# Optimization experiments

Hardware: AMD Instinct MI355X
Metric: run time of the kernel (lower is better)

Reference implementation:

```python
import jax, jax.numpy as jnp
import numpy as np

N, D_IN, H, L, K, Q = 131072, 384, 256, 32, 512, 4


def _lin_init(key, fan_in, fan_out):
    s = 1.0 / np.sqrt(fan_in)
    kw, kb = jax.random.split(key)
    w = jax.random.uniform(kw, (fan_in, fan_out), minval=-s, maxval=s, dtype=jnp.float32)
    b = jax.random.uniform(kb, (fan_out,), minval=-s, maxval=s, dtype=jnp.float32)
    return w, b


def setup_inputs() -> dict:
    key = jax.random.key(0)
    ks = jax.random.split(key, 8)
    enc_w1, enc_b1 = _lin_init(ks[1], D_IN, H)
    enc_w2, enc_b2 = _lin_init(ks[2], H, H)
    enc_w3, enc_b3 = _lin_init(ks[3], H, L)
    dec_w1, dec_b1 = _lin_init(ks[4], L, H)
    dec_w2, dec_b2 = _lin_init(ks[5], H, H)
    dec_w3, dec_b3 = _lin_init(ks[6], H, D_IN)
    codebooks = jax.random.normal(ks[7], (Q, K, L), dtype=jnp.float32) * 0.02
    x = jax.random.normal(ks[0], (N, D_IN), dtype=jnp.float32)
    return dict(x=x,
                enc_w1=enc_w1, enc_b1=enc_b1, enc_w2=enc_w2, enc_b2=enc_b2,
                enc_w3=enc_w3, enc_b3=enc_b3,
                dec_w1=dec_w1, dec_b1=dec_b1, dec_w2=dec_w2, dec_b2=dec_b2,
                dec_w3=dec_w3, dec_b3=dec_b3,
                codebooks=codebooks)


def _encoder(x, w1, b1, w2, b2, w3, b3):
    h = jax.nn.relu(x @ w1 + b1)
    h = jax.nn.relu(h @ w2 + b2)
    return h @ w3 + b3


def _decoder(z, w1, b1, w2, b2, w3, b3):
    h = jax.nn.relu(z @ w1 + b1)
    h = jax.nn.relu(h @ w2 + b2)
    return h @ w3 + b3


def _residual_vq(z, codebooks):
    """Residual VQ: Q stages of nearest-codeword lookup on the running residual.
    Returns (z_quantized with straight-through, indices [N,Q], commitment loss)."""
    residual = z
    quant_sum = jnp.zeros_like(z)
    indices = []
    commit = jnp.float32(0.0)
    for q in range(codebooks.shape[0]):  # small fixed loop over quantizer stages
        cb = codebooks[q]  # [K, L]
        # squared L2 distances [N, K] via expansion (cdist + argmin)
        d = (jnp.sum(residual * residual, axis=-1, keepdims=True)
             - 2.0 * residual @ cb.T
             + jnp.sum(cb * cb, axis=-1))
        idx = jnp.argmin(d, axis=-1)          # [N]
        qv = cb[idx]                          # gather [N, L]
        commit = commit + jnp.mean((jax.lax.stop_gradient(qv) - residual) ** 2)
        quant_sum = quant_sum + qv
        residual = residual - jax.lax.stop_gradient(qv)
        indices.append(idx)
    # straight-through estimator
    z_q = z + jax.lax.stop_gradient(quant_sum - z)
    return z_q, jnp.stack(indices, axis=-1), commit


def reference(x, enc_w1, enc_b1, enc_w2, enc_b2, enc_w3, enc_b3,
              dec_w1, dec_b1, dec_w2, dec_b2, dec_w3, dec_b3, codebooks):
    z = _encoder(x, enc_w1, enc_b1, enc_w2, enc_b2, enc_w3, enc_b3)
    z_q, indices, commit = _residual_vq(z, codebooks)
    x_recon = _decoder(z_q, dec_w1, dec_b1, dec_w2, dec_b2, dec_w3, dec_b3)
    return x_recon, indices, commit
```

## Files before the change

### kernel.cpp

```cpp
#include <hip/hip_runtime.h>
#include <hip/hip_bf16.h>
#include <math.h>


#define N_ROWS 131072
#define D_IN   384
#define H_DIM  256
#define L_DIM  32
#define K_CB   512
#define Q_ST   4
#define VQ_ROWS 256
#define NPART  (N_ROWS / VQ_ROWS)

typedef __attribute__((ext_vector_type(8))) short short8v;
typedef __attribute__((ext_vector_type(4))) float f32x4;

__device__ __forceinline__ ushort f2bf(float v)
{
    __hip_bfloat16 b = __float2bfloat16(v);
    return *reinterpret_cast<ushort*>(&b);
}

__device__ __forceinline__ float np_sumsq32(const float* __restrict__ v)
{
    #pragma clang fp contract(off)
    float s0 = v[0]*v[0], s1 = v[1]*v[1], s2 = v[2]*v[2], s3 = v[3]*v[3];
    float s4 = v[4]*v[4], s5 = v[5]*v[5], s6 = v[6]*v[6], s7 = v[7]*v[7];
    s0 = s0 + v[8]*v[8];   s1 = s1 + v[9]*v[9];   s2 = s2 + v[10]*v[10]; s3 = s3 + v[11]*v[11];
    s4 = s4 + v[12]*v[12]; s5 = s5 + v[13]*v[13]; s6 = s6 + v[14]*v[14]; s7 = s7 + v[15]*v[15];
    s0 = s0 + v[16]*v[16]; s1 = s1 + v[17]*v[17]; s2 = s2 + v[18]*v[18]; s3 = s3 + v[19]*v[19];
    s4 = s4 + v[20]*v[20]; s5 = s5 + v[21]*v[21]; s6 = s6 + v[22]*v[22]; s7 = s7 + v[23]*v[23];
    s0 = s0 + v[24]*v[24]; s1 = s1 + v[25]*v[25]; s2 = s2 + v[26]*v[26]; s3 = s3 + v[27]*v[27];
    s4 = s4 + v[28]*v[28]; s5 = s5 + v[29]*v[29]; s6 = s6 + v[30]*v[30]; s7 = s7 + v[31]*v[31];
    return ((s0 + s1) + (s2 + s3)) + ((s4 + s5) + (s6 + s7));
}

template<bool RELU>
__global__ __launch_bounds__(256)
void gemm_bias(const float* __restrict__ A, const float* __restrict__ B,
               const float* __restrict__ bias, float* __restrict__ C,
               int K, int Nout)
{
    #pragma clang fp contract(off)
    __shared__ float As2[32][132];
    __shared__ float Bs[32][128];
    const int t  = threadIdx.x;
    const int tc = t & 15;
    const int tr = t >> 4;
    const size_t row0 = (size_t)blockIdx.x * 128;
    const int    col0 = blockIdx.y * 128;

    float acc[8][8];
    #pragma unroll
    for (int i = 0; i < 8; ++i)
        #pragma unroll
        for (int j = 0; j < 8; ++j) acc[i][j] = 0.f;

    const int ar = t >> 3, ak = (t & 7) << 2;
    const int br = t >> 5, bc = (t & 31) << 2;

    for (int k0 = 0; k0 < K; k0 += 32) {
        #pragma unroll
        for (int i = 0; i < 4; ++i) {
            int r = ar + (i << 5);
            float4 v = *reinterpret_cast<const float4*>(A + (row0 + r) * (size_t)K + k0 + ak);
            As2[ak + 0][r] = v.x; As2[ak + 1][r] = v.y;
            As2[ak + 2][r] = v.z; As2[ak + 3][r] = v.w;
        }
        #pragma unroll
        for (int i = 0; i < 4; ++i) {
            int r = br + (i << 3);
            float4 v = *reinterpret_cast<const float4*>(B + (size_t)(k0 + r) * Nout + col0 + bc);
            *reinterpret_cast<float4*>(&Bs[r][bc]) = v;
        }
        __syncthreads();
        #pragma unroll
        for (int k = 0; k < 32; ++k) {
            float a[8], b[8];
            *reinterpret_cast<float4*>(&a[0]) = *reinterpret_cast<const float4*>(&As2[k][tr << 3]);
            *reinterpret_cast<float4*>(&a[4]) = *reinterpret_cast<const float4*>(&As2[k][(tr << 3) + 4]);
            *reinterpret_cast<float4*>(&b[0]) = *reinterpret_cast<const float4*>(&Bs[k][tc << 2]);
            *reinterpret_cast<float4*>(&b[4]) = *reinterpret_cast<const float4*>(&Bs[k][(tc << 2) + 64]);
            #pragma unroll
            for (int i = 0; i < 8; ++i)
                #pragma unroll
                for (int j = 0; j < 8; ++j) acc[i][j] = fmaf(a[i], b[j], acc[i][j]);
        }
        __syncthreads();
    }

    #pragma unroll
    for (int i = 0; i < 8; ++i) {
        size_t r = row0 + (tr << 3) + i;
        int c1 = col0 + (tc << 2);
        int c2 = c1 + 64;
        float v1[4], v2[4];
        #pragma unroll
        for (int j = 0; j < 4; ++j) {
            float u1 = acc[i][j]     + bias[c1 + j];
            float u2 = acc[i][j + 4] + bias[c2 + j];
            if (RELU) { u1 = fmaxf(u1, 0.0f); u2 = fmaxf(u2, 0.0f); }
            v1[j] = u1; v2[j] = u2;
        }
        *reinterpret_cast<float4*>(C + r * Nout + c1) = *reinterpret_cast<float4*>(&v1[0]);
        *reinterpret_cast<float4*>(C + r * Nout + c2) = *reinterpret_cast<float4*>(&v2[0]);
    }
}

__global__ __launch_bounds__(256)
void gemm_z(const float* __restrict__ A, const float* __restrict__ W,
            const float* __restrict__ bv, float* __restrict__ Z)
{
    #pragma clang fp contract(off)
    __shared__ float As2[32][132];
    __shared__ float Ws[32][36];
    const int t = threadIdx.x;
    const int cgz = t & 7, rgz = t >> 3;
    const size_t row0 = (size_t)blockIdx.x * 128;

    float acc[4][4];
    #pragma unroll
    for (int i = 0; i < 4; ++i)
        #pragma unroll
        for (int j = 0; j < 4; ++j) acc[i][j] = 0.f;

    const int ar = t >> 3, ak = (t & 7) << 2;
    for (int k0 = 0; k0 < H_DIM; k0 += 32) {
        #pragma unroll
        for (int i = 0; i < 4; ++i) {
            int r = ar + (i << 5);
            float4 v = *reinterpret_cast<const float4*>(A + (row0 + r) * (size_t)H_DIM + k0 + ak);
            As2[ak + 0][r] = v.x; As2[ak + 1][r] = v.y;
            As2[ak + 2][r] = v.z; As2[ak + 3][r] = v.w;
        }
        {
            int kr = t >> 3, cc = (t & 7) << 2;
            float4 v = *reinterpret_cast<const float4*>(W + (size_t)(k0 + kr) * L_DIM + cc);
            *reinterpret_cast<float4*>(&Ws[kr][cc]) = v;
        }
        __syncthreads();
        #pragma unroll
        for (int k = 0; k < 32; ++k) {
            float a[4], w[4];
            *reinterpret_cast<float4*>(&a[0]) = *reinterpret_cast<const float4*>(&As2[k][rgz << 2]);
            *reinterpret_cast<float4*>(&w[0]) = *reinterpret_cast<const float4*>(&Ws[k][cgz << 2]);
            #pragma unroll
            for (int i = 0; i < 4; ++i)
                #pragma unroll
                for (int j = 0; j < 4; ++j) acc[i][j] = fmaf(a[i], w[j], acc[i][j]);
        }
        __syncthreads();
    }
    #pragma unroll
    for (int i = 0; i < 4; ++i) {
        size_t row = row0 + (rgz << 2) + i;
        float v[4];
        #pragma unroll
        for (int j = 0; j < 4; ++j) v[j] = acc[i][j] + bv[(cgz << 2) + j];
        *reinterpret_cast<float4*>(Z + row * L_DIM + (cgz << 2)) = *reinterpret_cast<float4*>(&v[0]);
    }
}

__global__ __launch_bounds__(256)
void cnorm_kernel(const float* __restrict__ cbs, float* __restrict__ cnorm)
{
    #pragma clang fp contract(off)
    int g = blockIdx.x * 256 + threadIdx.x;
    const float* c = cbs + (size_t)g * L_DIM;
    float cl[L_DIM];
    #pragma unroll
    for (int l = 0; l < L_DIM; ++l) cl[l] = c[l];
    cnorm[g] = np_sumsq32(cl);
}

__global__ __launch_bounds__(256)
void prep_wt(const float* __restrict__ W, ushort* __restrict__ Wt, int K, int N)
{
    int g = blockIdx.x * 256 + threadIdx.x;
    if (g >= K * N) return;
    int n = g / K, k = g - n * K;
    Wt[g] = f2bf(W[(size_t)k * N + n]);
}

__global__ __launch_bounds__(256, 2)
void vq3_kernel(const float* __restrict__ zbuf, const float* __restrict__ cbs,
                const float* __restrict__ cnorm_g, ushort* __restrict__ zqb,
                float* __restrict__ idxOut, double* __restrict__ commitPart,
                int rowBase)
{
    #pragma clang fp contract(off)
    __shared__ float  cbL[K_CB * L_DIM];
    __shared__ float  cnL[K_CB];
    __shared__ double sred[256];

    const int t = threadIdx.x;
    const size_t lrow = (size_t)blockIdx.x * VQ_ROWS + t;
    const size_t grow = (size_t)rowBase + lrow;

    float z[L_DIM], r[L_DIM];
    {
        const float4* zp = reinterpret_cast<const float4*>(zbuf + lrow * L_DIM);
        #pragma unroll
        for (int j = 0; j < 8; ++j) {
            float4 v = zp[j];
            z[4*j+0]=v.x; z[4*j+1]=v.y; z[4*j+2]=v.z; z[4*j+3]=v.w;
        }
        #pragma unroll
        for (int l = 0; l < L_DIM; ++l) r[l] = z[l];
    }

    int bidx[Q_ST];
    double cAcc = 0.0;

    #pragma unroll 1
    for (int q = 0; q < Q_ST; ++q) {
        __syncthreads();
        {
            const float4* src = reinterpret_cast<const float4*>(cbs + (size_t)q * K_CB * L_DIM);
            float4* dst = reinterpret_cast<float4*>(cbL);
            #pragma unroll
            for (int i = 0; i < 16; ++i) dst[t + (i << 8)] = src[t + (i << 8)];
            cnL[t]       = cnorm_g[q * K_CB + t];
            cnL[t + 256] = cnorm_g[q * K_CB + t + 256];
        }
        __syncthreads();

        float rr = np_sumsq32(r);
        float bd = __builtin_inff();
        int   bi = 0;
        #pragma unroll 1
        for (int c = 0; c < K_CB; c += 2) {
            const float4* w0 = reinterpret_cast<const float4*>(cbL + (c << 5));
            const float4* w1 = w0 + 8;
            float a0 = 0.f, a1 = 0.f;
            #pragma unroll
            for (int j = 0; j < 8; ++j) {
                float4 u = w0[j], v = w1[j];
                a0 = fmaf(r[4*j+0], u.x, a0);  a1 = fmaf(r[4*j+0], v.x, a1);
                a0 = fmaf(r[4*j+1], u.y, a0);  a1 = fmaf(r[4*j+1], v.y, a1);
                a0 = fmaf(r[4*j+2], u.z, a0);  a1 = fmaf(r[4*j+2], v.z, a1);
                a0 = fmaf(r[4*j+3], u.w, a0);  a1 = fmaf(r[4*j+3], v.w, a1);
            }
            float d0 = (rr - 2.0f * a0) + cnL[c];
            float d1 = (rr - 2.0f * a1) + cnL[c + 1];
            if (d0 < bd) { bd = d0; bi = c; }
            if (d1 < bd) { bd = d1; bi = c + 1; }
        }
        bidx[q] = bi;

        {
            const float4* pw = reinterpret_cast<const float4*>(cbL + (bi << 5));
            float cs = 0.f;
            #pragma unroll
            for (int j = 0; j < 8; ++j) {
                float4 v = pw[j];
                float df;
                df = v.x - r[4*j+0]; cs = fmaf(df, df, cs); r[4*j+0] = r[4*j+0] - v.x;
                df = v.y - r[4*j+1]; cs = fmaf(df, df, cs); r[4*j+1] = r[4*j+1] - v.y;
                df = v.z - r[4*j+2]; cs = fmaf(df, df, cs); r[4*j+2] = r[4*j+2] - v.z;
                df = v.w - r[4*j+3]; cs = fmaf(df, df, cs); r[4*j+3] = r[4*j+3] - v.w;
            }
            cAcc += (double)cs;
        }
    }

    {
        float4 iv = make_float4((float)bidx[0], (float)bidx[1], (float)bidx[2], (float)bidx[3]);
        *reinterpret_cast<float4*>(idxOut + grow * Q_ST) = iv;
    }

    {
        ushort zq16[L_DIM];
        #pragma unroll
        for (int l = 0; l < L_DIM; ++l) zq16[l] = f2bf(z[l] - r[l]);
        uint4* o = reinterpret_cast<uint4*>(zqb + lrow * L_DIM);
        const uint4* s = reinterpret_cast<const uint4*>(zq16);
        #pragma unroll
        for (int j = 0; j < 4; ++j) o[j] = s[j];
    }

    sred[t] = cAcc;
    __syncthreads();
    for (int s = 128; s > 0; s >>= 1) {
        if (t < s) sred[t] += sred[t + s];
        __syncthreads();
    }
    if (t == 0) commitPart[rowBase / VQ_ROWS + blockIdx.x] = sred[0];
}

template<bool RELU, bool OUTBF16>
__global__ __launch_bounds__(256)
void mfma_gemm(const ushort* __restrict__ A, const ushort* __restrict__ Bt,
               const float* __restrict__ bias, void* __restrict__ Cout,
               int K, int Nout)
{
    __shared__ ushort As[128][40];
    __shared__ ushort Bs[128][40];
    const int t    = threadIdx.x;
    const int lane = t & 63;
    const int wid  = t >> 6;
    const int wr = wid >> 1, wc = wid & 1;
    const size_t row0 = (size_t)blockIdx.x * 128;
    const int    col0 = blockIdx.y * 128;

    f32x4 acc[4][4] = {};
    const int srow = t >> 1;
    const int sh   = (t & 1) << 4;

    for (int k0 = 0; k0 < K; k0 += 32) {
        {
            const ushort* ap = A + (row0 + srow) * (size_t)K + k0 + sh;
            uint4 v0 = *reinterpret_cast<const uint4*>(ap);
            uint4 v1 = *reinterpret_cast<const uint4*>(ap + 8);
            *reinterpret_cast<uint4*>(&As[srow][sh])     = v0;
            *reinterpret_cast<uint4*>(&As[srow][sh + 8]) = v1;
            const ushort* bp = Bt + (size_t)(col0 + srow) * K + k0 + sh;
            uint4 w0 = *reinterpret_cast<const uint4*>(bp);
            uint4 w1 = *reinterpret_cast<const uint4*>(bp + 8);
            *reinterpret_cast<uint4*>(&Bs[srow][sh])     = w0;
            *reinterpret_cast<uint4*>(&Bs[srow][sh + 8]) = w1;
        }
        __syncthreads();
        const int l15 = lane & 15, lk = (lane >> 4) << 3;
        short8v af[4], bf[4];
        #pragma unroll
        for (int f = 0; f < 4; ++f) {
            af[f] = *reinterpret_cast<const short8v*>(&As[(wr << 6) + (f << 4) + l15][lk]);
            bf[f] = *reinterpret_cast<const short8v*>(&Bs[(wc << 6) + (f << 4) + l15][lk]);
        }
        #pragma unroll
        for (int i = 0; i < 4; ++i)
            #pragma unroll
            for (int j = 0; j < 4; ++j)
                acc[i][j] = __builtin_amdgcn_mfma_f32_16x16x32_bf16(af[i], bf[j], acc[i][j], 0, 0, 0);
        __syncthreads();
    }

    const int l15 = lane & 15, lr4 = (lane >> 4) << 2;
    #pragma unroll
    for (int i = 0; i < 4; ++i) {
        #pragma unroll
        for (int j = 0; j < 4; ++j) {
            int col = col0 + (wc << 6) + (j << 4) + l15;
            float bv = bias[col];
            #pragma unroll
            for (int rj = 0; rj < 4; ++rj) {
                size_t row = row0 + (wr << 6) + (i << 4) + lr4 + rj;
                float v = acc[i][j][rj] + bv;
                if (RELU) v = fmaxf(v, 0.f);
                if (OUTBF16)
                    reinterpret_cast<ushort*>(Cout)[row * Nout + col] = f2bf(v);
                else
                    reinterpret_cast<float*>(Cout)[row * Nout + col] = v;
            }
        }
    }
}

__global__ __launch_bounds__(256)
void commit_finalize(const double* __restrict__ commitPart, float* __restrict__ outCommit)
{
    __shared__ double sred[256];
    const int t = threadIdx.x;
    double s = 0.0;
    for (int i = t; i < NPART; i += 256) s += commitPart[i];
    sred[t] = s;
    __syncthreads();
    for (int st = 128; st > 0; st >>= 1) {
        if (t < st) sred[t] += sred[t + st];
        __syncthreads();
    }
    if (t == 0)
        outCommit[0] = (float)(sred[0] / ((double)N_ROWS * (double)L_DIM));
}

extern "C" void kernel_launch(void* const* d_in, const int* in_sizes, int n_in,
                              void* d_out, int out_size, void* d_ws, size_t ws_size,
                              hipStream_t stream)
{
    const float* x      = (const float*)d_in[0];
    const float* enc_w1 = (const float*)d_in[1];
    const float* enc_b1 = (const float*)d_in[2];
    const float* enc_w2 = (const float*)d_in[3];
    const float* enc_b2 = (const float*)d_in[4];
    const float* enc_w3 = (const float*)d_in[5];
    const float* enc_b3 = (const float*)d_in[6];
    const float* dec_w1 = (const float*)d_in[7];
    const float* dec_b1 = (const float*)d_in[8];
    const float* dec_w2 = (const float*)d_in[9];
    const float* dec_b2 = (const float*)d_in[10];
    const float* dec_w3 = (const float*)d_in[11];
    const float* dec_b3 = (const float*)d_in[12];
    const float* cbs    = (const float*)d_in[13];

    float* out       = (float*)d_out;
    float* xrec      = out;
    float* idxOut    = out + (size_t)N_ROWS * D_IN;
    float* commitOut = idxOut + (size_t)N_ROWS * Q_ST;

    char*   wsb        = (char*)d_ws;
    float*  cnorm      = (float*)wsb;
    double* commitPart = (double*)(wsb + 8192);
    ushort* w1t        = (ushort*)(wsb + 12288);
    ushort* w2t        = (ushort*)(wsb + 28672);
    ushort* w3t        = (ushort*)(wsb + 159744);
    char*   bufs       = wsb + 360448;

    size_t availB = (ws_size > 360448) ? ws_size - 360448 : 0;
    long long chunk = (long long)(availB / 3264);
    chunk = (chunk / 256) * 256;
    if (chunk > N_ROWS) chunk = N_ROWS;
    if (chunk < 256) chunk = 256;

    float*  zbuf = (float*)bufs;
    float*  bufA = zbuf + (size_t)chunk * L_DIM;
    float*  bufB = bufA + (size_t)chunk * H_DIM;
    ushort* zqb  = (ushort*)(bufB + (size_t)chunk * H_DIM);
    ushort* h1b  = zqb + (size_t)chunk * L_DIM;
    ushort* h2b  = h1b + (size_t)chunk * H_DIM;

    cnorm_kernel<<<8, 256, 0, stream>>>(cbs, cnorm);
    prep_wt<<<(L_DIM  * H_DIM + 255) / 256, 256, 0, stream>>>(dec_w1, w1t, L_DIM, H_DIM);
    prep_wt<<<(H_DIM * H_DIM + 255) / 256, 256, 0, stream>>>(dec_w2, w2t, H_DIM, H_DIM);
    prep_wt<<<(H_DIM * D_IN + 255) / 256, 256, 0, stream>>>(dec_w3, w3t, H_DIM, D_IN);

    for (long long ro = 0; ro < N_ROWS; ro += chunk) {
        long long R = N_ROWS - ro;
        if (R > chunk) R = chunk;
        dim3 g2((unsigned)(R / 128), 2);
        dim3 g3((unsigned)(R / 128), 3);
        gemm_bias<true><<<g2, 256, 0, stream>>>(x + ro * D_IN, enc_w1, enc_b1, bufA, D_IN, H_DIM);
        gemm_bias<true><<<g2, 256, 0, stream>>>(bufA, enc_w2, enc_b2, bufB, H_DIM, H_DIM);
        gemm_z<<<(unsigned)(R / 128), 256, 0, stream>>>(bufB, enc_w3, enc_b3, zbuf);
        vq3_kernel<<<(unsigned)(R / VQ_ROWS), 256, 0, stream>>>(zbuf, cbs, cnorm, zqb,
                                                                idxOut, commitPart, (int)ro);
        mfma_gemm<true,  true ><<<g2, 256, 0, stream>>>(zqb, w1t, dec_b1, h1b, L_DIM, H_DIM);
        mfma_gemm<true,  true ><<<g2, 256, 0, stream>>>(h1b, w2t, dec_b2, h2b, H_DIM, H_DIM);
        mfma_gemm<false, false><<<g3, 256, 0, stream>>>(h2b, w3t, dec_b3, xrec + ro * D_IN, H_DIM, D_IN);
    }

    commit_finalize<<<1, 256, 0, stream>>>(commitPart, commitOut);
}
```

Before: 946.0 us.

## Register-prefetch next K tile in GEMMs and halve VQ codebook LDS footprint

Both the fp32 encoder GEMM and the bf16 MFMA decoder GEMM now load the next K-slice of A and B into registers right after the barrier, so global loads overlap the inner compute loop. The VQ kernel stages each codebook in two 256-entry halves, halving LDS use (from about 64KB to 32KB) and dropping the 2-wave occupancy hint to allow more blocks per CU. It also drops the saved copy of z, reading z back from global memory at the end and the chosen codeword from global memory. The costs are extra register pressure in the GEMMs, an extra barrier pair per VQ stage, and extra global reads in the VQ kernel.

```diff
diff --git a/kernel.cpp b/kernel.cpp
--- a/kernel.cpp
+++ b/kernel.cpp
@@ -59,21 +59,29 @@
     const int ar = t >> 3, ak = (t & 7) << 2;
     const int br = t >> 5, bc = (t & 31) << 2;
 
+    float4 Arg[4], Brg[4];
+    #pragma unroll
+    for (int i = 0; i < 4; ++i) {
+        Arg[i] = *reinterpret_cast<const float4*>(A + (row0 + ar + (i << 5)) * (size_t)K + ak);
+        Brg[i] = *reinterpret_cast<const float4*>(B + (size_t)(br + (i << 3)) * Nout + col0 + bc);
+    }
+
     for (int k0 = 0; k0 < K; k0 += 32) {
         #pragma unroll
         for (int i = 0; i < 4; ++i) {
             int r = ar + (i << 5);
-            float4 v = *reinterpret_cast<const float4*>(A + (row0 + r) * (size_t)K + k0 + ak);
-            As2[ak + 0][r] = v.x; As2[ak + 1][r] = v.y;
-            As2[ak + 2][r] = v.z; As2[ak + 3][r] = v.w;
-        }
-        #pragma unroll
-        for (int i = 0; i < 4; ++i) {
-            int r = br + (i << 3);
-            float4 v = *reinterpret_cast<const float4*>(B + (size_t)(k0 + r) * Nout + col0 + bc);
-            *reinterpret_cast<float4*>(&Bs[r][bc]) = v;
-        }
-        __syncthreads();
+            As2[ak + 0][r] = Arg[i].x; As2[ak + 1][r] = Arg[i].y;
+            As2[ak + 2][r] = Arg[i].z; As2[ak + 3][r] = Arg[i].w;
+            *reinterpret_cast<float4*>(&Bs[br + (i << 3)][bc]) = Brg[i];
+        }
+        __syncthreads();
+        if (k0 + 32 < K) {
+            #pragma unroll
+            for (int i = 0; i < 4; ++i) {
+                Arg[i] = *reinterpret_cast<const float4*>(A + (row0 + ar + (i << 5)) * (size_t)K + k0 + 32 + ak);
+                Brg[i] = *reinterpret_cast<const float4*>(B + (size_t)(k0 + 32 + br + (i << 3)) * Nout + col0 + bc);
+            }
+        }
         #pragma unroll
         for (int k = 0; k < 32; ++k) {
             float a[8], b[8];
@@ -182,14 +190,14 @@
     Wt[g] = f2bf(W[(size_t)k * N + n]);
 }
 
-__global__ __launch_bounds__(256, 2)
-void vq3_kernel(const float* __restrict__ zbuf, const float* __restrict__ cbs,
+__global__ __launch_bounds__(256)
+void vq4_kernel(const float* __restrict__ zbuf, const float* __restrict__ cbs,
                 const float* __restrict__ cnorm_g, ushort* __restrict__ zqb,
                 float* __restrict__ idxOut, double* __restrict__ commitPart,
                 int rowBase)
 {
     #pragma clang fp contract(off)
-    __shared__ float  cbL[K_CB * L_DIM];
+    __shared__ float  cbL[256 * L_DIM];
     __shared__ float  cnL[K_CB];
     __shared__ double sred[256];
 
@@ -197,16 +205,14 @@
     const size_t lrow = (size_t)blockIdx.x * VQ_ROWS + t;
     const size_t grow = (size_t)rowBase + lrow;
 
-    float z[L_DIM], r[L_DIM];
+    float r[L_DIM];
     {
         const float4* zp = reinterpret_cast<const float4*>(zbuf + lrow * L_DIM);
         #pragma unroll
         for (int j = 0; j < 8; ++j) {
             float4 v = zp[j];
-            z[4*j+0]=v.x; z[4*j+1]=v.y; z[4*j+2]=v.z; z[4*j+3]=v.w;
-        }
-        #pragma unroll
-        for (int l = 0; l < L_DIM; ++l) r[l] = z[l];
+            r[4*j+0]=v.x; r[4*j+1]=v.y; r[4*j+2]=v.z; r[4*j+3]=v.w;
+        }
     }
 
     int bidx[Q_ST];
@@ -214,42 +220,51 @@
 
     #pragma unroll 1
     for (int q = 0; q < Q_ST; ++q) {
-        __syncthreads();
-        {
-            const float4* src = reinterpret_cast<const float4*>(cbs + (size_t)q * K_CB * L_DIM);
-            float4* dst = reinterpret_cast<float4*>(cbL);
-            #pragma unroll
-            for (int i = 0; i < 16; ++i) dst[t + (i << 8)] = src[t + (i << 8)];
-            cnL[t]       = cnorm_g[q * K_CB + t];
-            cnL[t + 256] = cnorm_g[q * K_CB + t + 256];
-        }
-        __syncthreads();
+        const float4* cbq = reinterpret_cast<const float4*>(cbs + (size_t)q * K_CB * L_DIM);
 
         float rr = np_sumsq32(r);
         float bd = __builtin_inff();
         int   bi = 0;
+
         #pragma unroll 1
-        for (int c = 0; c < K_CB; c += 2) {
-            const float4* w0 = reinterpret_cast<const float4*>(cbL + (c << 5));
-            const float4* w1 = w0 + 8;
-            float a0 = 0.f, a1 = 0.f;
-            #pragma unroll
-            for (int j = 0; j < 8; ++j) {
-                float4 u = w0[j], v = w1[j];
-                a0 = fmaf(r[4*j+0], u.x, a0);  a1 = fmaf(r[4*j+0], v.x, a1);
-                a0 = fmaf(r[4*j+1], u.y, a0);  a1 = fmaf(r[4*j+1], v.y, a1);
-                a0 = fmaf(r[4*j+2], u.z, a0);  a1 = fmaf(r[4*j+2], v.z, a1);
-                a0 = fmaf(r[4*j+3], u.w, a0);  a1 = fmaf(r[4*j+3], v.w, a1);
+        for (int half = 0; half < 2; ++half) {
+            __syncthreads();
+            {
+                const float4* src = cbq + (half << 11);
+                float4* dst = reinterpret_cast<float4*>(cbL);
+                #pragma unroll
+                for (int i = 0; i < 8; ++i) dst[t + (i << 8)] = src[t + (i << 8)];
+                if (half == 0) {
+                    cnL[t]       = cnorm_g[q * K_CB + t];
+                    cnL[t + 256] = cnorm_g[q * K_CB + t + 256];
+                }
             }
-            float d0 = (rr - 2.0f * a0) + cnL[c];
-            float d1 = (rr - 2.0f * a1) + cnL[c + 1];
-            if (d0 < bd) { bd = d0; bi = c; }
-            if (d1 < bd) { bd = d1; bi = c + 1; }
+            __syncthreads();
+
+            const int cb0 = half << 8;
+            #pragma unroll 2
+            for (int c = 0; c < 256; c += 2) {
+                const float4* w0 = reinterpret_cast<const float4*>(cbL + (c << 5));
+                const float4* w1 = w0 + 8;
+                float a0 = 0.f, a1 = 0.f;
+                #pragma unroll
+                for (int j = 0; j < 8; ++j) {
+                    float4 u = w0[j], v = w1[j];
+                    a0 = fmaf(r[4*j+0], u.x, a0);  a1 = fmaf(r[4*j+0], v.x, a1);
+                    a0 = fmaf(r[4*j+1], u.y, a0);  a1 = fmaf(r[4*j+1], v.y, a1);
+                    a0 = fmaf(r[4*j+2], u.z, a0);  a1 = fmaf(r[4*j+2], v.z, a1);
+                    a0 = fmaf(r[4*j+3], u.w, a0);  a1 = fmaf(r[4*j+3], v.w, a1);
+                }
+                float d0 = (rr - 2.0f * a0) + cnL[cb0 + c];
+                float d1 = (rr - 2.0f * a1) + cnL[cb0 + c + 1];
+                if (d0 < bd) { bd = d0; bi = cb0 + c; }
+                if (d1 < bd) { bd = d1; bi = cb0 + c + 1; }
+            }
         }
         bidx[q] = bi;
 
         {
-            const float4* pw = reinterpret_cast<const float4*>(cbL + (bi << 5));
+            const float4* pw = cbq + ((size_t)bi << 3);
             float cs = 0.f;
             #pragma unroll
             for (int j = 0; j < 8; ++j) {
@@ -270,9 +285,16 @@
     }
 
     {
+        const float4* zp = reinterpret_cast<const float4*>(zbuf + lrow * L_DIM);
         ushort zq16[L_DIM];
         #pragma unroll
-        for (int l = 0; l < L_DIM; ++l) zq16[l] = f2bf(z[l] - r[l]);
+        for (int j = 0; j < 8; ++j) {
+            float4 v = zp[j];
+            zq16[4*j+0] = f2bf(v.x - r[4*j+0]);
+            zq16[4*j+1] = f2bf(v.y - r[4*j+1]);
+            zq16[4*j+2] = f2bf(v.z - r[4*j+2]);
+            zq16[4*j+3] = f2bf(v.w - r[4*j+3]);
+        }
         uint4* o = reinterpret_cast<uint4*>(zqb + lrow * L_DIM);
         const uint4* s = reinterpret_cast<const uint4*>(zq16);
         #pragma unroll
@@ -307,20 +329,30 @@
     const int srow = t >> 1;
     const int sh   = (t & 1) << 4;
 
+    uint4 av0, av1, bv0, bv1;
+    {
+        const ushort* ap = A + (row0 + srow) * (size_t)K + sh;
+        av0 = *reinterpret_cast<const uint4*>(ap);
+        av1 = *reinterpret_cast<const uint4*>(ap + 8);
+        const ushort* bp = Bt + (size_t)(col0 + srow) * K + sh;
+        bv0 = *reinterpret_cast<const uint4*>(bp);
+        bv1 = *reinterpret_cast<const uint4*>(bp + 8);
+    }
+
     for (int k0 = 0; k0 < K; k0 += 32) {
-        {
-            const ushort* ap = A + (row0 + srow) * (size_t)K + k0 + sh;
-            uint4 v0 = *reinterpret_cast<const uint4*>(ap);
-            uint4 v1 = *reinterpret_cast<const uint4*>(ap + 8);
-            *reinterpret_cast<uint4*>(&As[srow][sh])     = v0;
-            *reinterpret_cast<uint4*>(&As[srow][sh + 8]) = v1;
-            const ushort* bp = Bt + (size_t)(col0 + srow) * K + k0 + sh;
-            uint4 w0 = *reinterpret_cast<const uint4*>(bp);
-            uint4 w1 = *reinterpret_cast<const uint4*>(bp + 8);
-            *reinterpret_cast<uint4*>(&Bs[srow][sh])     = w0;
-            *reinterpret_cast<uint4*>(&Bs[srow][sh + 8]) = w1;
-        }
-        __syncthreads();
+        *reinterpret_cast<uint4*>(&As[srow][sh])     = av0;
+        *reinterpret_cast<uint4*>(&As[srow][sh + 8]) = av1;
+        *reinterpret_cast<uint4*>(&Bs[srow][sh])     = bv0;
+        *reinterpret_cast<uint4*>(&Bs[srow][sh + 8]) = bv1;
+        __syncthreads();
+        if (k0 + 32 < K) {
+            const ushort* ap = A + (row0 + srow) * (size_t)K + k0 + 32 + sh;
+            av0 = *reinterpret_cast<const uint4*>(ap);
+            av1 = *reinterpret_cast<const uint4*>(ap + 8);
+            const ushort* bp = Bt + (size_t)(col0 + srow) * K + k0 + 32 + sh;
+            bv0 = *reinterpret_cast<const uint4*>(bp);
+            bv1 = *reinterpret_cast<const uint4*>(bp + 8);
+        }
         const int l15 = lane & 15, lk = (lane >> 4) << 3;
         short8v af[4], bf[4];
         #pragma unroll
@@ -432,7 +464,7 @@
         gemm_bias<true><<<g2, 256, 0, stream>>>(x + ro * D_IN, enc_w1, enc_b1, bufA, D_IN, H_DIM);
         gemm_bias<true><<<g2, 256, 0, stream>>>(bufA, enc_w2, enc_b2, bufB, H_DIM, H_DIM);
         gemm_z<<<(unsigned)(R / 128), 256, 0, stream>>>(bufB, enc_w3, enc_b3, zbuf);
-        vq3_kernel<<<(unsigned)(R / VQ_ROWS), 256, 0, stream>>>(zbuf, cbs, cnorm, zqb,
+        vq4_kernel<<<(unsigned)(R / VQ_ROWS), 256, 0, stream>>>(zbuf, cbs, cnorm, zqb,
                                                                 idxOut, commitPart, (int)ro);
         mfma_gemm<true,  true ><<<g2, 256, 0, stream>>>(zqb, w1t, dec_b1, h1b, L_DIM, H_DIM);
         mfma_gemm<true,  true ><<<g2, 256, 0, stream>>>(h1b, w2t, dec_b2, h2b, H_DIM, H_DIM);
```

Measured after the change: 1.122 ms. +18.6%, slower.
